# Kernel tuning notes

Measured on AMD Instinct MI355X. Metric: run time of the kernel, lower is better.

The kernel has to match this reference:

```python
import jax, jax.numpy as jnp
import numpy as np

HIDDEN = 2048
N_HEADS = 32
N_KV_HEADS = 8
N_GROUPS = N_HEADS // N_KV_HEADS  # 4
HEAD_DIM = HIDDEN // N_HEADS      # 64
BATCH, SEQ = 2, 2048


def setup_inputs() -> dict:
    key = jax.random.key(0)
    ks = jax.random.split(key, 5)
    s = 0.02
    return {
        "x": jax.random.normal(ks[0], (BATCH, SEQ, HIDDEN), dtype=jnp.float32),
        "Wq": jax.random.normal(ks[1], (HIDDEN, HIDDEN), dtype=jnp.float32) * s,
        "Wk": jax.random.normal(ks[2], (N_KV_HEADS * HEAD_DIM, HIDDEN), dtype=jnp.float32) * s,
        "Wv": jax.random.normal(ks[3], (N_KV_HEADS * HEAD_DIM, HIDDEN), dtype=jnp.float32) * s,
        "Wo": jax.random.normal(ks[4], (HIDDEN, HIDDEN), dtype=jnp.float32) * s,
    }


def reference(x, Wq, Wk, Wv, Wo):
    b, s, _ = x.shape
    # Projections (nn.Linear: y = x @ W.T)
    q = (x @ Wq.T).reshape(b, s, N_KV_HEADS, N_GROUPS, HEAD_DIM)  # group heads by kv head
    k = (x @ Wk.T).reshape(b, s, N_KV_HEADS, HEAD_DIM)
    v = (x @ Wv.T).reshape(b, s, N_KV_HEADS, HEAD_DIM)
    scale = 1.0 / jnp.sqrt(jnp.asarray(HEAD_DIM, dtype=x.dtype))
    # Grouped scores: equivalent to repeat_interleave of K over groups
    scores = jnp.einsum('bqhgd,bkhd->bhgqk', q, k) * scale  # [b, kvh, g, s, s]
    causal_mask = jnp.triu(jnp.ones((s, s), dtype=bool), k=1)
    scores = jnp.where(causal_mask, -jnp.inf, scores)
    attn = jax.nn.softmax(scores, axis=-1)
    out = jnp.einsum('bhgqk,bkhd->bqhgd', attn, v)  # [b, s, kvh, g, hd]
    out = out.reshape(b, s, HIDDEN)
    return out @ Wo.T
```

## Files before the change

### kernel.cpp

```cpp
#include <hip/hip_runtime.h>

#define HIDDEN 2048
#define NHEADS 32
#define NKV 8
#define HD 64
#define BATCH 2
#define SEQ 2048
#define MROWS (BATCH*SEQ)
#define KVDIM (NKV*HD)
#define QKVN (HIDDEN + 2*KVDIM)

typedef __bf16 bf16x8 __attribute__((ext_vector_type(8)));
typedef float f32x4 __attribute__((ext_vector_type(4)));

__device__ inline void gld16(const __bf16* g, __bf16* l) {
    __builtin_amdgcn_global_load_lds((const __attribute__((address_space(1))) void*)g,
                                     (__attribute__((address_space(3))) void*)l, 16, 0, 0);
}

__global__ __launch_bounds__(256) void cast_all(const float* __restrict__ x,
                                                const float* __restrict__ wq,
                                                const float* __restrict__ wk,
                                                const float* __restrict__ wv,
                                                const float* __restrict__ wo,
                                                __bf16* __restrict__ xb,
                                                __bf16* __restrict__ wqkv,
                                                __bf16* __restrict__ wob,
                                                float qscale) {
    int blk = blockIdx.x;
    const float* src; __bf16* dst; float sc = 1.0f; size_t off;
    if (blk < 8192)        { src = x;  dst = xb;   off = (size_t)blk * 1024; }
    else if (blk < 12288)  { src = wq; dst = wqkv; off = (size_t)(blk - 8192) * 1024; sc = qscale; }
    else if (blk < 13312)  { src = wk; dst = wqkv + (size_t)HIDDEN * HIDDEN; off = (size_t)(blk - 12288) * 1024; }
    else if (blk < 14336)  { src = wv; dst = wqkv + (size_t)(HIDDEN + KVDIM) * HIDDEN; off = (size_t)(blk - 13312) * 1024; }
    else                   { src = wo; dst = wob;  off = (size_t)(blk - 14336) * 1024; }
    size_t i4 = off + (size_t)threadIdx.x * 4;
    float4 f = *(const float4*)(src + i4);
    dst[i4 + 0] = (__bf16)(f.x * sc);
    dst[i4 + 1] = (__bf16)(f.y * sc);
    dst[i4 + 2] = (__bf16)(f.z * sc);
    dst[i4 + 3] = (__bf16)(f.w * sc);
}

__device__ inline void store_val(__bf16* C, size_t idx, float v) { C[idx] = (__bf16)v; }
__device__ inline void store_val(float* C, size_t idx, float v) { C[idx] = v; }

template <typename OutT>
__global__ __launch_bounds__(256) void gemm128(const __bf16* __restrict__ A,
                                               const __bf16* __restrict__ B,
                                               OutT* __restrict__ C,
                                               int M, int N, int K) {
    __shared__ __bf16 As[2][128][32];
    __shared__ __bf16 Bs[2][128][32];
    const int tid  = threadIdx.x;
    const int lane = tid & 63;
    const int w    = tid >> 6;
    const int col  = lane & 15;
    const int quad = lane >> 4;
    const int m0 = blockIdx.y * 128;
    const int n0 = blockIdx.x * 128;
    const int wm = (w >> 1) * 64;
    const int wn = (w & 1) * 64;

    f32x4 acc[4][4];
    #pragma unroll
    for (int i = 0; i < 4; i++)
        #pragma unroll
        for (int j = 0; j < 4; j++) acc[i][j] = (f32x4){0.f,0.f,0.f,0.f};

    const int lrow = lane >> 2;
    const int lcol = (lane & 3) * 8;

    auto stage = [&](int k0, int buf) {
        #pragma unroll
        for (int c = 0; c < 4; c++) {
            int chunk = w * 4 + c;
            if (chunk < 8) {
                const __bf16* g = A + (size_t)(m0 + chunk*16 + lrow) * K + k0 + lcol;
                gld16(g, &As[buf][chunk*16][0]);
            } else {
                int bc = chunk - 8;
                const __bf16* g = B + (size_t)(n0 + bc*16 + lrow) * K + k0 + lcol;
                gld16(g, &Bs[buf][bc*16][0]);
            }
        }
    };

    const int nk = K / 32;
    stage(0, 0);
    for (int ki = 0; ki < nk; ki++) {
        const int buf = ki & 1;
        __syncthreads();
        if (ki + 1 < nk) stage((ki + 1) * 32, buf ^ 1);

        bf16x8 af[4], bfr[4];
        #pragma unroll
        for (int i = 0; i < 4; i++) af[i]  = *(const bf16x8*)&As[buf][wm + i*16 + col][quad*8];
        #pragma unroll
        for (int j = 0; j < 4; j++) bfr[j] = *(const bf16x8*)&Bs[buf][wn + j*16 + col][quad*8];
        #pragma unroll
        for (int i = 0; i < 4; i++)
            #pragma unroll
            for (int j = 0; j < 4; j++)
                acc[i][j] = __builtin_amdgcn_mfma_f32_16x16x32_bf16(af[i], bfr[j], acc[i][j], 0, 0, 0);
    }

    #pragma unroll
    for (int i = 0; i < 4; i++) {
        #pragma unroll
        for (int r = 0; r < 4; r++) {
            int mrow = m0 + wm + i*16 + quad*4 + r;
            size_t base = (size_t)mrow * N + n0 + wn;
            #pragma unroll
            for (int j = 0; j < 4; j++)
                store_val(C, base + j*16 + col, acc[i][j][r]);
        }
    }
}

__global__ __launch_bounds__(256) void transpose_v(const __bf16* __restrict__ QKV,
                                                   __bf16* __restrict__ VT) {
    __shared__ __bf16 tile[64][72];
    const int r0 = blockIdx.x * 64;
    const int s0 = blockIdx.y * 64;
    const int t  = threadIdx.x;
    #pragma unroll
    for (int cc = 0; cc < 2; cc++) {
        int c = t + cc * 256;
        int i = c >> 3;
        int j8 = (c & 7) * 8;
        bf16x8 v = *(const bf16x8*)(QKV + (size_t)(s0 + i) * QKVN + (HIDDEN + KVDIM) + r0 + j8);
        *(bf16x8*)&tile[i][j8] = v;
    }
    __syncthreads();
    #pragma unroll
    for (int cc = 0; cc < 2; cc++) {
        int c = t + cc * 256;
        int d = c >> 3;
        int sc = (c & 7) * 8;
        bf16x8 vv;
        #pragma unroll
        for (int j = 0; j < 8; j++) vv[j] = tile[sc + j][d];
        *(bf16x8*)(VT + (size_t)(r0 + d) * MROWS + s0 + sc) = vv;
    }
}

__global__ __launch_bounds__(256) void flash_attn(const __bf16* __restrict__ QKV,
                                                  const __bf16* __restrict__ VT,
                                                  __bf16* __restrict__ O) {
    const int bid  = blockIdx.x;
    const int p    = ((bid & 15) + 4 * ((bid >> 8) & 3)) & 15;
    const int head = (bid >> 4) & 31;
    const int b    = bid >> 9;
    const int kvh  = head >> 2;
    const int tid  = threadIdx.x;
    const int lane = tid & 63;
    const int w    = tid >> 6;
    const int col  = lane & 15;
    const int quad = lane >> 4;

    const int qbL = p * 64 + w * 16;
    const int qbH = (31 - p) * 64 + w * 16;
    const int np32 = (p + 1) * 2;
    const int nh32 = (32 - p) * 2;

    __shared__ __bf16 Ks[3][2][32][32];
    __shared__ __bf16 Vs[3][64][32];
    __shared__ __bf16 Pt[4][32][32];

    const size_t qL = (size_t)(b * SEQ + qbL + col) * QKVN + head * HD;
    const size_t qH = (size_t)(b * SEQ + qbH + col) * QKVN + head * HD;
    bf16x8 aqL0 = *(const bf16x8*)(QKV + qL + quad * 8);
    bf16x8 aqL1 = *(const bf16x8*)(QKV + qL + 32 + quad * 8);
    bf16x8 aqH0 = *(const bf16x8*)(QKV + qH + quad * 8);
    bf16x8 aqH1 = *(const bf16x8*)(QKV + qH + 32 + quad * 8);

    bf16x8 ones;
    #pragma unroll
    for (int j = 0; j < 8; j++) ones[j] = (__bf16)1.0f;

    f32x4 oL[4], oH[4];
    #pragma unroll
    for (int dn = 0; dn < 4; dn++) { oL[dn] = (f32x4){0.f,0.f,0.f,0.f}; oH[dn] = (f32x4){0.f,0.f,0.f,0.f}; }
    f32x4 lsumL = (f32x4){0.f,0.f,0.f,0.f};
    f32x4 lsumH = (f32x4){0.f,0.f,0.f,0.f};

    const int lrow = lane >> 2;
    const int srcc8 = (((lane & 3) ^ (lrow & 3)) * 8);
    const int swz   = (quad ^ (col & 3)) * 8;
    const int rswz  = (quad ^ (col & 3) ^ ((col >> 2) & 3)) * 8;
    const size_t bS = (size_t)b * SEQ;

    const __bf16 *g0, *g1;
    size_t gstep;
    if (w < 2) {
        g0 = QKV + (bS + lrow) * QKVN + HIDDEN + kvh * HD + w * 32 + srcc8;
        g1 = g0 + (size_t)16 * QKVN;
        gstep = (size_t)32 * QKVN;
    } else {
        g0 = VT + (size_t)(kvh * HD + (w - 2) * 32 + lrow) * MROWS + bS + srcc8;
        g1 = g0 + (size_t)16 * MROWS;
        gstep = 32;
    }

    auto stage = [&](int sb) {
        if (w < 2) {
            gld16(g0, &Ks[sb][w][0][0]);
            gld16(g1, &Ks[sb][w][16][0]);
        } else {
            gld16(g0, &Vs[sb][(w - 2) * 32][0]);
            gld16(g1, &Vs[sb][(w - 2) * 32 + 16][0]);
        }
        g0 += gstep; g1 += gstep;
    };

    stage(0);
    stage(1);
    int cur = 0, nx2 = 2;
    for (int kt = 0; kt < nh32; kt++) {
        const int kbase = kt * 32;
        const bool dual = (kt < np32);
        if (kt + 1 < nh32) { __asm__ volatile("s_waitcnt vmcnt(2)" ::: "memory"); }
        else               { __asm__ volatile("s_waitcnt vmcnt(0)" ::: "memory"); }
        __builtin_amdgcn_s_barrier();
        __asm__ volatile("" ::: "memory");
        if (kt + 2 < nh32) stage(nx2);

        f32x4 sH[2], sL[2];
        #pragma unroll
        for (int j = 0; j < 2; j++) { sH[j] = (f32x4){0.f,0.f,0.f,0.f}; sL[j] = (f32x4){0.f,0.f,0.f,0.f}; }
        __builtin_amdgcn_s_setprio(1);
        #pragma unroll
        for (int j = 0; j < 2; j++) {
            bf16x8 bk0 = *(const bf16x8*)&Ks[cur][0][j*16 + col][swz];
            bf16x8 bk1 = *(const bf16x8*)&Ks[cur][1][j*16 + col][swz];
            sH[j] = __builtin_amdgcn_mfma_f32_16x16x32_bf16(aqH0, bk0, sH[j], 0, 0, 0);
            sH[j] = __builtin_amdgcn_mfma_f32_16x16x32_bf16(aqH1, bk1, sH[j], 0, 0, 0);
            if (dual) {
                sL[j] = __builtin_amdgcn_mfma_f32_16x16x32_bf16(aqL0, bk0, sL[j], 0, 0, 0);
                sL[j] = __builtin_amdgcn_mfma_f32_16x16x32_bf16(aqL1, bk1, sL[j], 0, 0, 0);
            }
        }
        __builtin_amdgcn_s_setprio(0);

        if (kt >= nh32 - 2) {
            #pragma unroll
            for (int r = 0; r < 4; r++) {
                int qrow = qbH + quad*4 + r;
                #pragma unroll
                for (int j = 0; j < 2; j++)
                    if (kbase + j*16 + col > qrow) sH[j][r] = -1e30f;
            }
        }
        if (dual && kt >= np32 - 2) {
            #pragma unroll
            for (int r = 0; r < 4; r++) {
                int qrow = qbL + quad*4 + r;
                #pragma unroll
                for (int j = 0; j < 2; j++)
                    if (kbase + j*16 + col > qrow) sL[j][r] = -1e30f;
            }
        }

        #pragma unroll
        for (int r = 0; r < 4; r++) {
            int pr = quad*4 + r;
            #pragma unroll
            for (int j = 0; j < 2; j++) {
                int idx = (((j*2 + (col >> 3)) ^ r ^ quad) * 8) + (col & 7);
                Pt[w][pr][idx] = (__bf16)__builtin_amdgcn_exp2f(sH[j][r]);
            }
        }
        if (dual) {
            #pragma unroll
            for (int r = 0; r < 4; r++) {
                int pr = quad*4 + r;
                #pragma unroll
                for (int j = 0; j < 2; j++) {
                    int idx = (((j*2 + (col >> 3)) ^ r ^ quad) * 8) + (col & 7);
                    Pt[w][16 + pr][idx] = (__bf16)__builtin_amdgcn_exp2f(sL[j][r]);
                }
            }
        }

        __asm__ volatile("s_waitcnt lgkmcnt(0)" ::: "memory");
        bf16x8 apH = *(const bf16x8*)&Pt[w][col][rswz];
        __builtin_amdgcn_s_setprio(1);
        lsumH = __builtin_amdgcn_mfma_f32_16x16x32_bf16(apH, ones, lsumH, 0, 0, 0);
        bf16x8 apL;
        if (dual) {
            apL = *(const bf16x8*)&Pt[w][16 + col][rswz];
            lsumL = __builtin_amdgcn_mfma_f32_16x16x32_bf16(apL, ones, lsumL, 0, 0, 0);
        }

        #pragma unroll
        for (int dn = 0; dn < 4; dn++) {
            bf16x8 bv = *(const bf16x8*)&Vs[cur][dn*16 + col][swz];
            oH[dn] = __builtin_amdgcn_mfma_f32_16x16x32_bf16(apH, bv, oH[dn], 0, 0, 0);
            if (dual)
                oL[dn] = __builtin_amdgcn_mfma_f32_16x16x32_bf16(apL, bv, oL[dn], 0, 0, 0);
        }
        __builtin_amdgcn_s_setprio(0);

        cur = (cur == 2) ? 0 : cur + 1;
        nx2 = (nx2 == 2) ? 0 : nx2 + 1;
    }

    #pragma unroll
    for (int r = 0; r < 4; r++) {
        float invL = 1.0f / lsumL[r];
        float invH = 1.0f / lsumH[r];
        __bf16* opL = O + (size_t)(b * SEQ + qbL + quad*4 + r) * HIDDEN + head * HD;
        __bf16* opH = O + (size_t)(b * SEQ + qbH + quad*4 + r) * HIDDEN + head * HD;
        #pragma unroll
        for (int dn = 0; dn < 4; dn++) {
            opL[dn*16 + col] = (__bf16)(oL[dn][r] * invL);
            opH[dn*16 + col] = (__bf16)(oH[dn][r] * invH);
        }
    }
}

extern "C" void kernel_launch(void* const* d_in, const int* in_sizes, int n_in,
                              void* d_out, int out_size, void* d_ws, size_t ws_size,
                              hipStream_t stream) {
    const float* x  = (const float*)d_in[0];
    const float* Wq = (const float*)d_in[1];
    const float* Wk = (const float*)d_in[2];
    const float* Wv = (const float*)d_in[3];
    const float* Wo = (const float*)d_in[4];
    float* out = (float*)d_out;

    __bf16* p    = (__bf16*)d_ws;
    __bf16* xb   = p; p += (size_t)MROWS * HIDDEN;
    __bf16* wqkv = p; p += (size_t)QKVN * HIDDEN;
    __bf16* wob  = p; p += (size_t)HIDDEN * HIDDEN;
    __bf16* qkv  = p; p += (size_t)MROWS * QKVN;
    __bf16* vt   = p; p += (size_t)KVDIM * MROWS;
    __bf16* aob  = xb;

    const float qscale = 0.125f * 1.4426950408889634f;
    cast_all<<<18432, 256, 0, stream>>>(x, Wq, Wk, Wv, Wo, xb, wqkv, wob, qscale);

    dim3 blk(256);
    gemm128<__bf16><<<dim3(QKVN/128, MROWS/128), blk, 0, stream>>>(xb, wqkv, qkv, MROWS, QKVN, HIDDEN);
    transpose_v<<<dim3(KVDIM/64, MROWS/64), blk, 0, stream>>>(qkv, vt);
    flash_attn<<<BATCH * NHEADS * (SEQ/128), blk, 0, stream>>>(qkv, vt, aob);
    gemm128<float><<<dim3(HIDDEN/128, MROWS/128), blk, 0, stream>>>(aob, wob, out, MROWS, HIDDEN, HIDDEN);
}
```

Baseline: 335.1 us.

## Keep softmax probabilities in registers by computing transposed scores

Swaps the MFMA operand order so the score tile comes out transposed, letting the exponentiated probabilities feed the P·V MFMA straight from registers through 16x16x16 bf16 instructions. This removes the per-tile LDS round trip for P (store, lgkmcnt wait, reload). To match, V^T is written with a permuted column order and the swizzle on the V LDS loads is dropped. The cost is twice as many smaller MFMAs for P·V and row sums, and the unswizzled V reads may cause LDS bank conflicts.

```diff
diff --git a/kernel.cpp b/kernel.cpp
--- a/kernel.cpp
+++ b/kernel.cpp
@@ -11,7 +11,17 @@
 #define QKVN (HIDDEN + 2*KVDIM)
 
 typedef __bf16 bf16x8 __attribute__((ext_vector_type(8)));
+typedef __bf16 bf16x4 __attribute__((ext_vector_type(4)));
 typedef float f32x4 __attribute__((ext_vector_type(4)));
+typedef short s16x4 __attribute__((ext_vector_type(4)));
+typedef short s16x8 __attribute__((ext_vector_type(8)));
+
+__device__ inline f32x4 mfma32(bf16x8 a, bf16x8 b, f32x4 c) {
+    return __builtin_amdgcn_mfma_f32_16x16x32_bf16(a, b, c, 0, 0, 0);
+}
+__device__ inline f32x4 mfma16(s16x4 a, s16x4 b, f32x4 c) {
+    return __builtin_amdgcn_mfma_f32_16x16x16bf16_1k(a, b, c, 0, 0, 0);
+}
 
 __device__ inline void gld16(const __bf16* g, __bf16* l) {
     __builtin_amdgcn_global_load_lds((const __attribute__((address_space(1))) void*)g,
@@ -137,11 +147,14 @@
     for (int cc = 0; cc < 2; cc++) {
         int c = t + cc * 256;
         int d = c >> 3;
-        int sc = (c & 7) * 8;
+        int m = c & 7;
         bf16x8 vv;
         #pragma unroll
-        for (int j = 0; j < 8; j++) vv[j] = tile[sc + j][d];
-        *(bf16x8*)(VT + (size_t)(r0 + d) * MROWS + s0 + sc) = vv;
+        for (int tt = 0; tt < 8; tt++) {
+            int sl = (m >> 2) * 32 + (tt >> 2) * 16 + (m & 3) * 4 + (tt & 3);
+            vv[tt] = tile[sl][d];
+        }
+        *(bf16x8*)(VT + (size_t)(r0 + d) * MROWS + s0 + m * 8) = vv;
     }
 }
 
@@ -166,7 +179,6 @@
 
     __shared__ __bf16 Ks[3][2][32][32];
     __shared__ __bf16 Vs[3][64][32];
-    __shared__ __bf16 Pt[4][32][32];
 
     const size_t qL = (size_t)(b * SEQ + qbL + col) * QKVN + head * HD;
     const size_t qH = (size_t)(b * SEQ + qbH + col) * QKVN + head * HD;
@@ -175,9 +187,7 @@
     bf16x8 aqH0 = *(const bf16x8*)(QKV + qH + quad * 8);
     bf16x8 aqH1 = *(const bf16x8*)(QKV + qH + 32 + quad * 8);
 
-    bf16x8 ones;
-    #pragma unroll
-    for (int j = 0; j < 8; j++) ones[j] = (__bf16)1.0f;
+    const s16x4 ones4 = { (short)0x3F80, (short)0x3F80, (short)0x3F80, (short)0x3F80 };
 
     f32x4 oL[4], oH[4];
     #pragma unroll
@@ -188,7 +198,6 @@
     const int lrow = lane >> 2;
     const int srcc8 = (((lane & 3) ^ (lrow & 3)) * 8);
     const int swz   = (quad ^ (col & 3)) * 8;
-    const int rswz  = (quad ^ (col & 3) ^ ((col >> 2) & 3)) * 8;
     const size_t bS = (size_t)b * SEQ;
 
     const __bf16 *g0, *g1;
@@ -198,7 +207,7 @@
         g1 = g0 + (size_t)16 * QKVN;
         gstep = (size_t)32 * QKVN;
     } else {
-        g0 = VT + (size_t)(kvh * HD + (w - 2) * 32 + lrow) * MROWS + bS + srcc8;
+        g0 = VT + (size_t)(kvh * HD + (w - 2) * 32 + lrow) * MROWS + bS + (lane & 3) * 8;
         g1 = g0 + (size_t)16 * MROWS;
         gstep = 32;
     }
@@ -234,71 +243,62 @@
         for (int j = 0; j < 2; j++) {
             bf16x8 bk0 = *(const bf16x8*)&Ks[cur][0][j*16 + col][swz];
             bf16x8 bk1 = *(const bf16x8*)&Ks[cur][1][j*16 + col][swz];
-            sH[j] = __builtin_amdgcn_mfma_f32_16x16x32_bf16(aqH0, bk0, sH[j], 0, 0, 0);
-            sH[j] = __builtin_amdgcn_mfma_f32_16x16x32_bf16(aqH1, bk1, sH[j], 0, 0, 0);
+            sH[j] = mfma32(bk0, aqH0, sH[j]);
+            sH[j] = mfma32(bk1, aqH1, sH[j]);
             if (dual) {
-                sL[j] = __builtin_amdgcn_mfma_f32_16x16x32_bf16(aqL0, bk0, sL[j], 0, 0, 0);
-                sL[j] = __builtin_amdgcn_mfma_f32_16x16x32_bf16(aqL1, bk1, sL[j], 0, 0, 0);
+                sL[j] = mfma32(bk0, aqL0, sL[j]);
+                sL[j] = mfma32(bk1, aqL1, sL[j]);
             }
         }
         __builtin_amdgcn_s_setprio(0);
 
         if (kt >= nh32 - 2) {
             #pragma unroll
-            for (int r = 0; r < 4; r++) {
-                int qrow = qbH + quad*4 + r;
+            for (int j = 0; j < 2; j++)
                 #pragma unroll
-                for (int j = 0; j < 2; j++)
-                    if (kbase + j*16 + col > qrow) sH[j][r] = -1e30f;
+                for (int r = 0; r < 4; r++)
+                    if (kbase + j*16 + quad*4 + r > qbH + col) sH[j][r] = -1e30f;
+        }
+        if (dual && kt >= np32 - 2) {
+            #pragma unroll
+            for (int j = 0; j < 2; j++)
+                #pragma unroll
+                for (int r = 0; r < 4; r++)
+                    if (kbase + j*16 + quad*4 + r > qbL + col) sL[j][r] = -1e30f;
+        }
+
+        s16x4 paH[2], paL[2];
+        #pragma unroll
+        for (int j = 0; j < 2; j++) {
+            bf16x4 tb;
+            #pragma unroll
+            for (int r = 0; r < 4; r++) tb[r] = (__bf16)__builtin_amdgcn_exp2f(sH[j][r]);
+            paH[j] = __builtin_bit_cast(s16x4, tb);
+            lsumH = mfma16(paH[j], ones4, lsumH);
+        }
+        if (dual) {
+            #pragma unroll
+            for (int j = 0; j < 2; j++) {
+                bf16x4 tb;
+                #pragma unroll
+                for (int r = 0; r < 4; r++) tb[r] = (__bf16)__builtin_amdgcn_exp2f(sL[j][r]);
+                paL[j] = __builtin_bit_cast(s16x4, tb);
+                lsumL = mfma16(paL[j], ones4, lsumL);
             }
         }
-        if (dual && kt >= np32 - 2) {
-            #pragma unroll
-            for (int r = 0; r < 4; r++) {
-                int qrow = qbL + quad*4 + r;
-                #pragma unroll
-                for (int j = 0; j < 2; j++)
-                    if (kbase + j*16 + col > qrow) sL[j][r] = -1e30f;
+
+        __builtin_amdgcn_s_setprio(1);
+        #pragma unroll
+        for (int dn = 0; dn < 4; dn++) {
+            s16x8 bvv = *(const s16x8*)&Vs[cur][dn*16 + col][quad*8];
+            s16x4 bv0 = __builtin_shufflevector(bvv, bvv, 0, 1, 2, 3);
+            s16x4 bv1 = __builtin_shufflevector(bvv, bvv, 4, 5, 6, 7);
+            oH[dn] = mfma16(paH[0], bv0, oH[dn]);
+            oH[dn] = mfma16(paH[1], bv1, oH[dn]);
+            if (dual) {
+                oL[dn] = mfma16(paL[0], bv0, oL[dn]);
+                oL[dn] = mfma16(paL[1], bv1, oL[dn]);
             }
-        }
-
-        #pragma unroll
-        for (int r = 0; r < 4; r++) {
-            int pr = quad*4 + r;
-            #pragma unroll
-            for (int j = 0; j < 2; j++) {
-                int idx = (((j*2 + (col >> 3)) ^ r ^ quad) * 8) + (col & 7);
-                Pt[w][pr][idx] = (__bf16)__builtin_amdgcn_exp2f(sH[j][r]);
-            }
-        }
-        if (dual) {
-            #pragma unroll
-            for (int r = 0; r < 4; r++) {
-                int pr = quad*4 + r;
-                #pragma unroll
-                for (int j = 0; j < 2; j++) {
-                    int idx = (((j*2 + (col >> 3)) ^ r ^ quad) * 8) + (col & 7);
-                    Pt[w][16 + pr][idx] = (__bf16)__builtin_amdgcn_exp2f(sL[j][r]);
-                }
-            }
-        }
-
-        __asm__ volatile("s_waitcnt lgkmcnt(0)" ::: "memory");
-        bf16x8 apH = *(const bf16x8*)&Pt[w][col][rswz];
-        __builtin_amdgcn_s_setprio(1);
-        lsumH = __builtin_amdgcn_mfma_f32_16x16x32_bf16(apH, ones, lsumH, 0, 0, 0);
-        bf16x8 apL;
-        if (dual) {
-            apL = *(const bf16x8*)&Pt[w][16 + col][rswz];
-            lsumL = __builtin_amdgcn_mfma_f32_16x16x32_bf16(apL, ones, lsumL, 0, 0, 0);
-        }
-
-        #pragma unroll
-        for (int dn = 0; dn < 4; dn++) {
-            bf16x8 bv = *(const bf16x8*)&Vs[cur][dn*16 + col][swz];
-            oH[dn] = __builtin_amdgcn_mfma_f32_16x16x32_bf16(apH, bv, oH[dn], 0, 0, 0);
-            if (dual)
-                oL[dn] = __builtin_amdgcn_mfma_f32_16x16x32_bf16(apL, bv, oL[dn], 0, 0, 0);
         }
         __builtin_amdgcn_s_setprio(0);
 
```

Result: faster. 312.7 us (-6.7%).
